# Performance work log

Hardware: AMD Instinct MI355X
Metric: run time of the kernel (lower is better)

The kernel has to match this reference:

```python
import jax, jax.numpy as jnp
import numpy as np

N_NODES = 20000
N_EDGES = 320000
N_GRAPHS = 200
MAX_NODES = 100


def gcn_conv(x, W, b, src, dst, n_nodes):
    # PyG GCNConv: linear transform, add self-loops, symmetric normalization
    h = x @ W                                   # [N, out]
    loop = jnp.arange(n_nodes)
    s = jnp.concatenate([src, loop])
    d = jnp.concatenate([dst, loop])
    deg = jax.ops.segment_sum(jnp.ones_like(s, dtype=h.dtype), d, num_segments=n_nodes)
    dinv = jax.lax.rsqrt(jnp.maximum(deg, 1.0))  # deg >= 1 due to self-loops
    norm = dinv[s] * dinv[d]                     # [E+N]
    msg = h[s] * norm[:, None]                   # gather + scale
    return jax.ops.segment_sum(msg, d, num_segments=n_nodes) + b


def setup_inputs() -> dict:
    key = jax.random.key(0)
    ks = jax.random.split(key, 16)
    IN, H, L = 128, 256, 64
    P = MAX_NODES * (MAX_NODES - 1) // 2
    inp = {
        "x": jax.random.normal(ks[0], (N_NODES, IN), jnp.float32),
        "edge_index": jax.random.randint(ks[1], (2, N_EDGES), 0, N_NODES),
        "batch": jnp.sort(jax.random.randint(ks[2], (N_NODES,), 0, N_GRAPHS)),
        "eps": jax.random.normal(ks[3], (N_GRAPHS, L), jnp.float32),
        "W1": jax.random.normal(ks[4], (IN, H), jnp.float32) * (1.0 / np.sqrt(IN)),
        "b1": jnp.zeros((H,), jnp.float32),
        "W2": jax.random.normal(ks[5], (H, H), jnp.float32) * (1.0 / np.sqrt(H)),
        "b2": jnp.zeros((H,), jnp.float32),
        "Wmu": jax.random.normal(ks[6], (H, L), jnp.float32) * (1.0 / np.sqrt(H)),
        "bmu": jnp.zeros((L,), jnp.float32),
        "Wlv": jax.random.normal(ks[7], (H, L), jnp.float32) * (1.0 / np.sqrt(H)),
        "blv": jnp.zeros((L,), jnp.float32),
        "D1": jax.random.normal(ks[8], (L, H), jnp.float32) * (1.0 / np.sqrt(L)),
        "db1": jnp.zeros((H,), jnp.float32),
        "D2": jax.random.normal(ks[9], (H, H), jnp.float32) * (1.0 / np.sqrt(H)),
        "db2": jnp.zeros((H,), jnp.float32),
        "D3": jax.random.normal(ks[10], (H, P), jnp.float32) * (1.0 / np.sqrt(H)),
        "db3": jnp.zeros((P,), jnp.float32),
    }
    return inp


def reference(x, edge_index, batch, eps, W1, b1, W2, b2, Wmu, bmu, Wlv, blv,
              D1, db1, D2, db2, D3, db3):
    src, dst = edge_index[0], edge_index[1]
    # encoder
    h = jax.nn.relu(gcn_conv(x, W1, b1, src, dst, N_NODES))
    h = jax.nn.relu(gcn_conv(h, W2, b2, src, dst, N_NODES))
    # global mean pool
    sums = jax.ops.segment_sum(h, batch, num_segments=N_GRAPHS)
    cnt = jax.ops.segment_sum(jnp.ones((N_NODES,), h.dtype), batch, num_segments=N_GRAPHS)
    hg = sums / jnp.maximum(cnt, 1.0)[:, None]   # [B, H]
    mu = hg @ Wmu + bmu
    logvar = hg @ Wlv + blv
    # reparameterise
    z = mu + eps * jnp.exp(0.5 * logvar)
    # decoder MLP
    d = jax.nn.relu(z @ D1 + db1)
    d = jax.nn.relu(d @ D2 + db2)
    probs = jax.nn.sigmoid(d @ D3 + db3)         # [B, MAX_NODES*(MAX_NODES-1)//2]
    iu, ju = jnp.triu_indices(MAX_NODES, k=1)
    B = z.shape[0]
    adj = jnp.zeros((B, MAX_NODES, MAX_NODES), probs.dtype)
    adj = adj.at[:, iu, ju].set(probs)
    adj = adj + jnp.swapaxes(adj, 1, 2)
    return adj, mu, logvar
```

## Files before the change

### kernel.cpp

```cpp
#include <hip/hip_runtime.h>
#include <math.h>

#define N_NODES  20000
#define N_EDGES  320000
#define N_GRAPHS 200
#define MAXN     100
#define F_IN     128
#define F_H      256
#define F_L      64
#define P_PAIRS  4950
#define P_PAD    4992
#define ADJ_SIZE (N_GRAPHS * MAXN * MAXN)
#define MU_OFF   ADJ_SIZE
#define LV_OFF   (ADJ_SIZE + N_GRAPHS * F_L)

#define ELL_W    64
#define EF_NB    ((N_EDGES + 255) / 256)

static inline int ceil_div(int a, int b) { return (a + b - 1) / b; }

typedef __attribute__((ext_vector_type(8))) short bf16x8;
typedef __attribute__((ext_vector_type(4))) float f32x4;

static __device__ inline unsigned short f2bf(float f) {
    union { float f; unsigned u; } v; v.f = f;
    unsigned r = (v.u + 0x7FFFu + ((v.u >> 16) & 1u)) >> 16;
    return (unsigned short)r;
}
static __device__ inline float bf2f(unsigned short s) {
    union { unsigned u; float f; } v; v.u = (unsigned)s << 16; return v.f;
}
static __device__ inline float4 ubf4(ushort4 u) {
    float4 f;
    f.x = bf2f(u.x); f.y = bf2f(u.y); f.z = bf2f(u.z); f.w = bf2f(u.w);
    return f;
}
static __device__ inline float rdeg(int d) { return rsqrtf((float)d + 1.0f); }

#define PP_S1  32768
#define PP_S2  98304
#define PP_END 1376256
#define PP_NB  (PP_END / 256)
#define CV_END 640000
#define CV_NB  (CV_END / 256)
__global__ __launch_bounds__(256) void k_prep(
        const int* __restrict__ src, const int* __restrict__ dst,
        int* __restrict__ fill, int* __restrict__ ell,
        const float* __restrict__ W1, const float* __restrict__ W2,
        const float* __restrict__ D3,
        unsigned short* __restrict__ W1p, unsigned short* __restrict__ W2p,
        unsigned short* __restrict__ D3p,
        const float* __restrict__ x, unsigned short* __restrict__ xs) {
    if (blockIdx.x < EF_NB) {
        int e = blockIdx.x * 256 + threadIdx.x;
        if (e < N_EDGES) {
            int d = dst[e];
            int pos = atomicAdd(fill + d, 1);
            if (pos < ELL_W) ell[d * ELL_W + pos] = src[e];
        }
        return;
    }
    if (blockIdx.x < EF_NB + PP_NB) {
        int pid = (blockIdx.x - EF_NB) * 256 + threadIdx.x;
        const float* W; unsigned short* Bp; int N, NP, t;
        if (pid < PP_S1)      { t = pid;          W = W1; Bp = W1p; N = 256;     NP = 256; }
        else if (pid < PP_S2) { t = pid - PP_S1;  W = W2; Bp = W2p; N = 256;     NP = 256; }
        else                  { t = pid - PP_S2;  W = D3; Bp = D3p; N = P_PAIRS; NP = P_PAD; }
        int j    = t & 7;
        int lane = (t >> 3) & 63;
        int tile = t >> 9;
        int NT = NP >> 4;
        int nt = tile % NT;
        int kt = tile / NT;
        int k = kt * 32 + (lane >> 4) * 8 + j;
        int n = nt * 16 + (lane & 15);
        Bp[t] = (n < N) ? f2bf(W[(size_t)k * N + n]) : (unsigned short)0;
        return;
    }
    int tid = (blockIdx.x - EF_NB - PP_NB) * 256 + threadIdx.x;
    if (tid >= CV_END) return;
    float4 val = ((const float4*)x)[tid];
    ushort4 o;
    o.x = f2bf(val.x); o.y = f2bf(val.y);
    o.z = f2bf(val.z); o.w = f2bf(val.w);
    ((ushort4*)xs)[tid] = o;
}

__global__ __launch_bounds__(512) void k_layer1(const unsigned short* __restrict__ xs,
                                                const int* __restrict__ fill,
                                                const int* __restrict__ ell,
                                                const unsigned short* __restrict__ W1p,
                                                const float* __restrict__ bias,
                                                unsigned short* __restrict__ h1s, int M) {
    __shared__ unsigned short At[32 * 128];
    char* Ab = (char*)At;
    const int tid  = threadIdx.x;
    const int lane = tid & 63;
    const int w    = tid >> 6;

    for (int s = 0; s < 4; ++s) {
        int slot = w * 4 + s;
        int v = blockIdx.x * 32 + slot;
        ushort2 ob; ob.x = 0; ob.y = 0;
        if (v < M) {
            int dg  = fill[v];
            int beg = v * ELL_W;
            int end = beg + min(dg, ELL_W);
            float dv = rdeg(dg);
            float2 a0 = make_float2(0.f, 0.f), a1 = make_float2(0.f, 0.f);
            int i = beg;
            for (; i + 8 <= end; i += 8) {
                int s0 = ell[i + 0], s1 = ell[i + 1], s2 = ell[i + 2], s3 = ell[i + 3];
                int s4 = ell[i + 4], s5 = ell[i + 5], s6 = ell[i + 6], s7 = ell[i + 7];
                float r0 = rdeg(fill[s0]), r1 = rdeg(fill[s1]);
                float r2 = rdeg(fill[s2]), r3 = rdeg(fill[s3]);
                float r4 = rdeg(fill[s4]), r5 = rdeg(fill[s5]);
                float r6 = rdeg(fill[s6]), r7 = rdeg(fill[s7]);
                ushort2 u0 = ((const ushort2*)(xs + (size_t)s0 * F_IN))[lane];
                ushort2 u1 = ((const ushort2*)(xs + (size_t)s1 * F_IN))[lane];
                ushort2 u2 = ((const ushort2*)(xs + (size_t)s2 * F_IN))[lane];
                ushort2 u3 = ((const ushort2*)(xs + (size_t)s3 * F_IN))[lane];
                ushort2 u4 = ((const ushort2*)(xs + (size_t)s4 * F_IN))[lane];
                ushort2 u5 = ((const ushort2*)(xs + (size_t)s5 * F_IN))[lane];
                ushort2 u6 = ((const ushort2*)(xs + (size_t)s6 * F_IN))[lane];
                ushort2 u7 = ((const ushort2*)(xs + (size_t)s7 * F_IN))[lane];
                a0.x += r0 * bf2f(u0.x) + r2 * bf2f(u2.x) + r4 * bf2f(u4.x) + r6 * bf2f(u6.x);
                a0.y += r0 * bf2f(u0.y) + r2 * bf2f(u2.y) + r4 * bf2f(u4.y) + r6 * bf2f(u6.y);
                a1.x += r1 * bf2f(u1.x) + r3 * bf2f(u3.x) + r5 * bf2f(u5.x) + r7 * bf2f(u7.x);
                a1.y += r1 * bf2f(u1.y) + r3 * bf2f(u3.y) + r5 * bf2f(u5.y) + r7 * bf2f(u7.y);
            }
            for (; i + 4 <= end; i += 4) {
                int s0 = ell[i + 0], s1 = ell[i + 1], s2 = ell[i + 2], s3 = ell[i + 3];
                float r0 = rdeg(fill[s0]), r1 = rdeg(fill[s1]);
                float r2 = rdeg(fill[s2]), r3 = rdeg(fill[s3]);
                ushort2 u0 = ((const ushort2*)(xs + (size_t)s0 * F_IN))[lane];
                ushort2 u1 = ((const ushort2*)(xs + (size_t)s1 * F_IN))[lane];
                ushort2 u2 = ((const ushort2*)(xs + (size_t)s2 * F_IN))[lane];
                ushort2 u3 = ((const ushort2*)(xs + (size_t)s3 * F_IN))[lane];
                a0.x += r0 * bf2f(u0.x) + r2 * bf2f(u2.x);
                a0.y += r0 * bf2f(u0.y) + r2 * bf2f(u2.y);
                a1.x += r1 * bf2f(u1.x) + r3 * bf2f(u3.x);
                a1.y += r1 * bf2f(u1.y) + r3 * bf2f(u3.y);
            }
            for (; i < end; ++i) {
                int sv = ell[i];
                float rr = rdeg(fill[sv]);
                ushort2 u = ((const ushort2*)(xs + (size_t)sv * F_IN))[lane];
                a0.x += rr * bf2f(u.x); a0.y += rr * bf2f(u.y);
            }
            ushort2 uv = ((const ushort2*)(xs + (size_t)v * F_IN))[lane];
            ob.x = f2bf(dv * (a0.x + a1.x + dv * bf2f(uv.x)));
            ob.y = f2bf(dv * (a0.y + a1.y + dv * bf2f(uv.y)));
        }
        int byteoff = (slot * 256 + lane * 4) ^ ((slot & 7) << 4);
        *(ushort2*)(Ab + byteoff) = ob;
    }
    __syncthreads();

    const int rowhalf = w >> 2;
    const int colgrp  = w & 3;
    const int quad = lane >> 4;
    const int l15  = lane & 15;
    const int ar = rowhalf * 16 + l15;

    f32x4 acc[4];
    #pragma unroll
    for (int nt = 0; nt < 4; ++nt) acc[nt] = (f32x4){0.f, 0.f, 0.f, 0.f};

    #pragma unroll
    for (int kt = 0; kt < 4; ++kt) {
        int c = kt * 64 + quad * 16;
        bf16x8 a0 = *(const bf16x8*)(Ab + ((ar * 256 + c) ^ ((ar & 7) << 4)));
        #pragma unroll
        for (int nt = 0; nt < 4; ++nt) {
            bf16x8 b = *(const bf16x8*)(W1p + (((size_t)kt * 16 + colgrp * 4 + nt) * 64 + lane) * 8);
            acc[nt] = __builtin_amdgcn_mfma_f32_16x16x32_bf16(a0, b, acc[nt], 0, 0, 0);
        }
    }

    #pragma unroll
    for (int r = 0; r < 4; ++r) {
        int gm = blockIdx.x * 32 + rowhalf * 16 + quad * 4 + r;
        if (gm >= M) continue;
        float dv = rdeg(fill[gm]);
        #pragma unroll
        for (int nt = 0; nt < 4; ++nt) {
            int gn = colgrp * 64 + nt * 16 + l15;
            float s = acc[nt][r] + bias[gn];
            h1s[(size_t)gm * F_H + gn] = f2bf(fmaxf(s, 0.0f) * dv);
        }
    }
}

__global__ __launch_bounds__(512) void k_layer2(const unsigned short* __restrict__ h1s,
                                                const int* __restrict__ fill,
                                                const int* __restrict__ ell,
                                                const unsigned short* __restrict__ W2p,
                                                const float* __restrict__ bias,
                                                const int* __restrict__ batch,
                                                float* __restrict__ hg, int M) {
    __shared__ __align__(16) char smem[32 * 260 * 4];
    __shared__ int gb[32];
    char* Ab = smem;
    const int tid  = threadIdx.x;
    const int lane = tid & 63;
    const int w    = tid >> 6;

    if (tid < 32) {
        int gm = blockIdx.x * 32 + tid;
        gb[tid] = (gm < M) ? batch[gm] : -1;
    }

    for (int s = 0; s < 4; ++s) {
        int slot = w * 4 + s;
        int v = blockIdx.x * 32 + slot;
        ushort4 ob; ob.x = ob.y = ob.z = ob.w = 0;
        if (v < M) {
            int dg  = fill[v];
            int beg = v * ELL_W;
            int end = beg + min(dg, ELL_W);
            float4 a0 = make_float4(0.f, 0.f, 0.f, 0.f);
            float4 a1 = make_float4(0.f, 0.f, 0.f, 0.f);
            int i = beg;
            for (; i + 8 <= end; i += 8) {
                int s0 = ell[i + 0], s1 = ell[i + 1], s2 = ell[i + 2], s3 = ell[i + 3];
                int s4 = ell[i + 4], s5 = ell[i + 5], s6 = ell[i + 6], s7 = ell[i + 7];
                float4 h0 = ubf4(((const ushort4*)(h1s + (size_t)s0 * F_H))[lane]);
                float4 h1 = ubf4(((const ushort4*)(h1s + (size_t)s1 * F_H))[lane]);
                float4 h2 = ubf4(((const ushort4*)(h1s + (size_t)s2 * F_H))[lane]);
                float4 h3 = ubf4(((const ushort4*)(h1s + (size_t)s3 * F_H))[lane]);
                float4 h4 = ubf4(((const ushort4*)(h1s + (size_t)s4 * F_H))[lane]);
                float4 h5 = ubf4(((const ushort4*)(h1s + (size_t)s5 * F_H))[lane]);
                float4 h6 = ubf4(((const ushort4*)(h1s + (size_t)s6 * F_H))[lane]);
                float4 h7 = ubf4(((const ushort4*)(h1s + (size_t)s7 * F_H))[lane]);
                a0.x += h0.x + h2.x + h4.x + h6.x; a0.y += h0.y + h2.y + h4.y + h6.y;
                a0.z += h0.z + h2.z + h4.z + h6.z; a0.w += h0.w + h2.w + h4.w + h6.w;
                a1.x += h1.x + h3.x + h5.x + h7.x; a1.y += h1.y + h3.y + h5.y + h7.y;
                a1.z += h1.z + h3.z + h5.z + h7.z; a1.w += h1.w + h3.w + h5.w + h7.w;
            }
            for (; i + 4 <= end; i += 4) {
                int s0 = ell[i + 0], s1 = ell[i + 1], s2 = ell[i + 2], s3 = ell[i + 3];
                float4 h0 = ubf4(((const ushort4*)(h1s + (size_t)s0 * F_H))[lane]);
                float4 h1 = ubf4(((const ushort4*)(h1s + (size_t)s1 * F_H))[lane]);
                float4 h2 = ubf4(((const ushort4*)(h1s + (size_t)s2 * F_H))[lane]);
                float4 h3 = ubf4(((const ushort4*)(h1s + (size_t)s3 * F_H))[lane]);
                a0.x += h0.x + h2.x; a0.y += h0.y + h2.y; a0.z += h0.z + h2.z; a0.w += h0.w + h2.w;
                a1.x += h1.x + h3.x; a1.y += h1.y + h3.y; a1.z += h1.z + h3.z; a1.w += h1.w + h3.w;
            }
            for (; i < end; ++i) {
                int sv = ell[i];
                float4 h = ubf4(((const ushort4*)(h1s + (size_t)sv * F_H))[lane]);
                a0.x += h.x; a0.y += h.y; a0.z += h.z; a0.w += h.w;
            }
            float dv = rdeg(dg);
            float4 hv = ubf4(((const ushort4*)(h1s + (size_t)v * F_H))[lane]);
            ob.x = f2bf(dv * (a0.x + a1.x + hv.x));
            ob.y = f2bf(dv * (a0.y + a1.y + hv.y));
            ob.z = f2bf(dv * (a0.z + a1.z + hv.z));
            ob.w = f2bf(dv * (a0.w + a1.w + hv.w));
        }
        int byteoff = (slot * 512 + lane * 8) ^ ((slot & 7) << 4);
        *(ushort4*)(Ab + byteoff) = ob;
    }
    __syncthreads();

    const int rowhalf = w >> 2;
    const int colgrp  = w & 3;
    const int quad = lane >> 4;
    const int l15  = lane & 15;
    const int ar = rowhalf * 16 + l15;

    f32x4 acc[4];
    #pragma unroll
    for (int nt = 0; nt < 4; ++nt) acc[nt] = (f32x4){0.f, 0.f, 0.f, 0.f};

    #pragma unroll
    for (int kt = 0; kt < 8; ++kt) {
        int cb = kt * 64 + quad * 16;
        bf16x8 a0 = *(const bf16x8*)(Ab + ((ar * 512 + cb) ^ ((ar & 7) << 4)));
        #pragma unroll
        for (int nt = 0; nt < 4; ++nt) {
            bf16x8 b = *(const bf16x8*)(W2p + (((size_t)kt * 16 + colgrp * 4 + nt) * 64 + lane) * 8);
            acc[nt] = __builtin_amdgcn_mfma_f32_16x16x32_bf16(a0, b, acc[nt], 0, 0, 0);
        }
    }
    __syncthreads();

    float* sm = (float*)smem;
    #pragma unroll
    for (int r = 0; r < 4; ++r) {
        int wrow = rowhalf * 16 + quad * 4 + r;
        #pragma unroll
        for (int nt = 0; nt < 4; ++nt) {
            int cl = colgrp * 64 + nt * 16 + l15;
            sm[wrow * 260 + cl] = fmaxf(acc[nt][r] + bias[cl], 0.0f);
        }
    }
    __syncthreads();

    int c  = tid & 255;
    int r0 = (tid >> 8) * 16;
    float s = 0.0f;
    int cur = gb[r0];
    #pragma unroll 4
    for (int r = 0; r < 16; ++r) {
        int g = gb[r0 + r];
        if (g != cur) {
            if (cur >= 0) atomicAdd(hg + (size_t)cur * F_H + c, s);
            s = 0.0f; cur = g;
        }
        s += sm[(r0 + r) * 260 + c];
    }
    if (cur >= 0) atomicAdd(hg + (size_t)cur * F_H + c, s);
}

__global__ __launch_bounds__(512) void k_head_dec(const float* __restrict__ hg,
                                                  const int* __restrict__ batch,
                                                  const float* __restrict__ Wmu,
                                                  const float* __restrict__ bmu,
                                                  const float* __restrict__ Wlv,
                                                  const float* __restrict__ blv,
                                                  const float* __restrict__ eps,
                                                  const float* __restrict__ D1,
                                                  const float* __restrict__ db1,
                                                  const float* __restrict__ D2,
                                                  const float* __restrict__ db2,
                                                  float* __restrict__ out,
                                                  unsigned short* __restrict__ d2b) {
    int g = blockIdx.x;
    int tid = threadIdx.x;
    __shared__ float hgs[F_H];
    __shared__ float pp[512];
    __shared__ float mulv[128];
    __shared__ float zs[F_L];
    __shared__ float d1s[F_H];
    __shared__ float sInv;
    if (tid == 0) {
        int lo = 0, hi = N_NODES;
        while (lo < hi) { int mid = (lo + hi) >> 1; if (batch[mid] < g) lo = mid + 1; else hi = mid; }
        int beg = lo;
        hi = N_NODES;
        while (lo < hi) { int mid = (lo + hi) >> 1; if (batch[mid] < g + 1) lo = mid + 1; else hi = mid; }
        sInv = 1.0f / fmaxf((float)(lo - beg), 1.0f);
    }
    __syncthreads();
    if (tid < F_H) hgs[tid] = hg[(size_t)g * F_H + tid] * sInv;
    __syncthreads();
    {
        int o = tid & 127;
        int q = tid >> 7;
        int l = o & 63;
        const float* W = (o < 64) ? Wmu : Wlv;
        float s = 0.0f;
        int k0 = q * 64;
        #pragma unroll 8
        for (int k = k0; k < k0 + 64; ++k) s += hgs[k] * W[(size_t)k * F_L + l];
        pp[tid] = s;
    }
    __syncthreads();
    if (tid < 128) {
        int l = tid & 63;
        float s = pp[tid] + pp[tid + 128] + pp[tid + 256] + pp[tid + 384]
                + ((tid < 64) ? bmu[l] : blv[l]);
        out[((tid < 64) ? MU_OFF : LV_OFF) + g * F_L + l] = s;
        mulv[tid] = s;
    }
    __syncthreads();
    if (tid < 64)
        zs[tid] = mulv[tid] + eps[g * F_L + tid] * expf(0.5f * mulv[64 + tid]);
    __syncthreads();
    {
        int o = tid & 255;
        int h = tid >> 8;
        float s = 0.0f;
        int k0 = h * 32;
        #pragma unroll 8
        for (int k = k0; k < k0 + 32; ++k) s += zs[k] * D1[(size_t)k * F_H + o];
        pp[tid] = s;
    }
    __syncthreads();
    if (tid < 256) d1s[tid] = fmaxf(pp[tid] + pp[tid + 256] + db1[tid], 0.0f);
    __syncthreads();
    {
        int o = tid & 255;
        int h = tid >> 8;
        float s = 0.0f;
        int k0 = h * 128;
        #pragma unroll 8
        for (int k = k0; k < k0 + 128; ++k) s += d1s[k] * D2[(size_t)k * F_H + o];
        pp[tid] = s;
    }
    __syncthreads();
    if (tid < 256)
        d2b[(size_t)g * F_H + tid] = f2bf(fmaxf(pp[tid] + pp[tid + 256] + db2[tid], 0.0f));
}

__global__ __launch_bounds__(256) void k_gemm3(const unsigned short* __restrict__ A,
                                               const unsigned short* __restrict__ Bp,
                                               float* __restrict__ Y,
                                               const float* __restrict__ bias,
                                               int M, int N, int NP) {
    constexpr int KT = F_H / 32;
    const int NT   = NP >> 4;
    const int lane = threadIdx.x & 63;
    const int wave = threadIdx.x >> 6;
    const int bm   = blockIdx.y * 32;
    const int ng   = blockIdx.x * 4 + wave;
    const int quad = lane >> 4;
    const int l15  = lane & 15;

    int m0 = bm + l15;
    int m1 = m0 + 16;
    int m0c = min(m0, M - 1), m1c = min(m1, M - 1);

    f32x4 acc[2];
    acc[0] = (f32x4){0.f, 0.f, 0.f, 0.f};
    acc[1] = (f32x4){0.f, 0.f, 0.f, 0.f};

    #pragma unroll
    for (int kt = 0; kt < KT; ++kt) {
        bf16x8 a0 = *(const bf16x8*)(A + (size_t)m0c * F_H + kt * 32 + quad * 8);
        bf16x8 a1 = *(const bf16x8*)(A + (size_t)m1c * F_H + kt * 32 + quad * 8);
        bf16x8 b = *(const bf16x8*)(Bp + (((size_t)kt * NT + ng) * 64 + lane) * 8);
        acc[0] = __builtin_amdgcn_mfma_f32_16x16x32_bf16(a0, b, acc[0], 0, 0, 0);
        acc[1] = __builtin_amdgcn_mfma_f32_16x16x32_bf16(a1, b, acc[1], 0, 0, 0);
    }

    #pragma unroll
    for (int i = 0; i < 2; ++i) {
        #pragma unroll
        for (int r = 0; r < 4; ++r) {
            int gm = bm + i * 16 + quad * 4 + r;
            if (gm >= M) continue;
            int gn = (ng << 4) + l15;
            if (gn >= N) continue;
            float s = acc[i][r] + bias[gn];
            Y[(size_t)gm * N + gn] = 1.0f / (1.0f + expf(-s));
        }
    }
}

__global__ __launch_bounds__(256) void k_adj(const float* __restrict__ probs,
                                             float* __restrict__ adj) {
    int i = blockIdx.x * blockDim.x + threadIdx.x;
    if (i >= N_GRAPHS * MAXN * (MAXN / 4)) return;
    int b4 = (i % (MAXN / 4)) * 4;
    int a  = (i / (MAXN / 4)) % MAXN;
    int g  = i / (MAXN * (MAXN / 4));
    const float* pg = probs + (size_t)g * P_PAIRS;
    float4 o;
    float* op = (float*)&o;
    #pragma unroll
    for (int c = 0; c < 4; ++c) {
        int b = b4 + c;
        float v = 0.0f;
        if (a != b) {
            int lo = min(a, b), hi = max(a, b);
            int p = lo * (MAXN - 1) - (lo * (lo - 1)) / 2 + (hi - lo - 1);
            v = pg[p];
        }
        op[c] = v;
    }
    ((float4*)adj)[i] = o;
}

extern "C" void kernel_launch(void* const* d_in, const int* in_sizes, int n_in,
                              void* d_out, int out_size, void* d_ws, size_t ws_size,
                              hipStream_t stream) {
    const float* x    = (const float*)d_in[0];
    const int*   eidx = (const int*)d_in[1];
    const int*   batch= (const int*)d_in[2];
    const float* eps  = (const float*)d_in[3];
    const float* W1   = (const float*)d_in[4];
    const float* b1   = (const float*)d_in[5];
    const float* W2   = (const float*)d_in[6];
    const float* b2   = (const float*)d_in[7];
    const float* Wmu  = (const float*)d_in[8];
    const float* bmu  = (const float*)d_in[9];
    const float* Wlv  = (const float*)d_in[10];
    const float* blv  = (const float*)d_in[11];
    const float* D1   = (const float*)d_in[12];
    const float* db1  = (const float*)d_in[13];
    const float* D2   = (const float*)d_in[14];
    const float* db2  = (const float*)d_in[15];
    const float* D3   = (const float*)d_in[16];
    const float* db3  = (const float*)d_in[17];

    const int* src = eidx;
    const int* dst = eidx + N_EDGES;
    float* out = (float*)d_out;

    char* wsb = (char*)d_ws;
    size_t o = 0;
    auto carve = [&](size_t bytes) { void* p = wsb + o; o += (bytes + 255) & ~255ull; return p; };
    int*   fill   = (int*)  carve(N_NODES * sizeof(int));
    float* hg     = (float*)carve((size_t)N_GRAPHS * F_H * sizeof(float));
    int*   ell    = (int*)  carve((size_t)N_NODES * ELL_W * sizeof(int));
    unsigned short* xs  = (unsigned short*)carve((size_t)N_NODES * F_IN * sizeof(short));
    unsigned short* W1p = (unsigned short*)carve((size_t)F_IN * F_H * sizeof(short));
    unsigned short* W2p = (unsigned short*)carve((size_t)F_H * F_H * sizeof(short));
    unsigned short* D3p = (unsigned short*)carve((size_t)F_H * P_PAD * sizeof(short));
    unsigned short* h1s = (unsigned short*)carve((size_t)N_NODES * F_H * sizeof(short));
    unsigned short* d2b = (unsigned short*)carve((size_t)N_GRAPHS * F_H * sizeof(short));
    float* probs  = (float*)carve((size_t)N_GRAPHS * P_PAIRS * sizeof(float));

    hipMemsetAsync(fill, 0, 284928, stream);
    k_prep<<<EF_NB + PP_NB + CV_NB, 256, 0, stream>>>(src, dst, fill, ell,
                                                      W1, W2, D3, W1p, W2p, D3p,
                                                      x, xs);

    k_layer1<<<ceil_div(N_NODES, 32), 512, 0, stream>>>(xs, fill, ell,
                                                        W1p, b1, h1s, N_NODES);

    k_layer2<<<ceil_div(N_NODES, 32), 512, 0, stream>>>(h1s, fill, ell,
                                                        W2p, b2, batch, hg, N_NODES);

    k_head_dec<<<N_GRAPHS, 512, 0, stream>>>(hg, batch, Wmu, bmu, Wlv, blv, eps,
                                             D1, db1, D2, db2, out, d2b);

    {
        dim3 grid(P_PAD / 64, ceil_div(N_GRAPHS, 32));
        k_gemm3<<<grid, 256, 0, stream>>>(d2b, D3p, probs, db3,
                                          N_GRAPHS, P_PAIRS, P_PAD);
    }

    k_adj<<<ceil_div(N_GRAPHS * MAXN * (MAXN / 4), 256), 256, 0, stream>>>(probs, out);
}
```

Before: 207.6 us.

## Halve node tile per block in GCN layers to 16 rows and store pooled rows as bf16

Layer1 and layer2 now handle 16 nodes per 512-thread block instead of 32, doubling the grid. Each wave gathers 2 nodes instead of 4 and computes a 16x32 output slice with 2 MFMA accumulators. This trades more blocks and more repeated weight-fragment loads for shorter per-block gather latency and better load balance across CUs. Layer2 also stages the ReLU output in LDS as bf16 with a 272-short row stride, so the shared buffer shrinks. This adds rounding before the mean-pool atomics.

```diff
diff --git a/kernel.cpp b/kernel.cpp
--- a/kernel.cpp
+++ b/kernel.cpp
@@ -92,15 +92,15 @@
                                                 const unsigned short* __restrict__ W1p,
                                                 const float* __restrict__ bias,
                                                 unsigned short* __restrict__ h1s, int M) {
-    __shared__ unsigned short At[32 * 128];
+    __shared__ unsigned short At[16 * 128];
     char* Ab = (char*)At;
     const int tid  = threadIdx.x;
     const int lane = tid & 63;
     const int w    = tid >> 6;
 
-    for (int s = 0; s < 4; ++s) {
-        int slot = w * 4 + s;
-        int v = blockIdx.x * 32 + slot;
+    for (int s = 0; s < 2; ++s) {
+        int slot = w * 2 + s;
+        int v = blockIdx.x * 16 + slot;
         ushort2 ob; ob.x = 0; ob.y = 0;
         if (v < M) {
             int dg  = fill[v];
@@ -157,35 +157,33 @@
     }
     __syncthreads();
 
-    const int rowhalf = w >> 2;
-    const int colgrp  = w & 3;
     const int quad = lane >> 4;
     const int l15  = lane & 15;
-    const int ar = rowhalf * 16 + l15;
-
-    f32x4 acc[4];
-    #pragma unroll
-    for (int nt = 0; nt < 4; ++nt) acc[nt] = (f32x4){0.f, 0.f, 0.f, 0.f};
+    const int ar = l15;
+
+    f32x4 acc[2];
+    acc[0] = (f32x4){0.f, 0.f, 0.f, 0.f};
+    acc[1] = (f32x4){0.f, 0.f, 0.f, 0.f};
 
     #pragma unroll
     for (int kt = 0; kt < 4; ++kt) {
         int c = kt * 64 + quad * 16;
         bf16x8 a0 = *(const bf16x8*)(Ab + ((ar * 256 + c) ^ ((ar & 7) << 4)));
         #pragma unroll
-        for (int nt = 0; nt < 4; ++nt) {
-            bf16x8 b = *(const bf16x8*)(W1p + (((size_t)kt * 16 + colgrp * 4 + nt) * 64 + lane) * 8);
+        for (int nt = 0; nt < 2; ++nt) {
+            bf16x8 b = *(const bf16x8*)(W1p + (((size_t)kt * 16 + w * 2 + nt) * 64 + lane) * 8);
             acc[nt] = __builtin_amdgcn_mfma_f32_16x16x32_bf16(a0, b, acc[nt], 0, 0, 0);
         }
     }
 
     #pragma unroll
     for (int r = 0; r < 4; ++r) {
-        int gm = blockIdx.x * 32 + rowhalf * 16 + quad * 4 + r;
+        int gm = blockIdx.x * 16 + quad * 4 + r;
         if (gm >= M) continue;
         float dv = rdeg(fill[gm]);
         #pragma unroll
-        for (int nt = 0; nt < 4; ++nt) {
-            int gn = colgrp * 64 + nt * 16 + l15;
+        for (int nt = 0; nt < 2; ++nt) {
+            int gn = w * 32 + nt * 16 + l15;
             float s = acc[nt][r] + bias[gn];
             h1s[(size_t)gm * F_H + gn] = f2bf(fmaxf(s, 0.0f) * dv);
         }
@@ -199,21 +197,21 @@
                                                 const float* __restrict__ bias,
                                                 const int* __restrict__ batch,
                                                 float* __restrict__ hg, int M) {
-    __shared__ __align__(16) char smem[32 * 260 * 4];
-    __shared__ int gb[32];
+    __shared__ __align__(16) char smem[16 * 272 * 2];
+    __shared__ int gb[16];
     char* Ab = smem;
     const int tid  = threadIdx.x;
     const int lane = tid & 63;
     const int w    = tid >> 6;
 
-    if (tid < 32) {
-        int gm = blockIdx.x * 32 + tid;
+    if (tid < 16) {
+        int gm = blockIdx.x * 16 + tid;
         gb[tid] = (gm < M) ? batch[gm] : -1;
     }
 
-    for (int s = 0; s < 4; ++s) {
-        int slot = w * 4 + s;
-        int v = blockIdx.x * 32 + slot;
+    for (int s = 0; s < 2; ++s) {
+        int slot = w * 2 + s;
+        int v = blockIdx.x * 16 + slot;
         ushort4 ob; ob.x = ob.y = ob.z = ob.w = 0;
         if (v < M) {
             int dg  = fill[v];
@@ -264,52 +262,50 @@
     }
     __syncthreads();
 
-    const int rowhalf = w >> 2;
-    const int colgrp  = w & 3;
     const int quad = lane >> 4;
     const int l15  = lane & 15;
-    const int ar = rowhalf * 16 + l15;
-
-    f32x4 acc[4];
-    #pragma unroll
-    for (int nt = 0; nt < 4; ++nt) acc[nt] = (f32x4){0.f, 0.f, 0.f, 0.f};
+    const int ar = l15;
+
+    f32x4 acc[2];
+    acc[0] = (f32x4){0.f, 0.f, 0.f, 0.f};
+    acc[1] = (f32x4){0.f, 0.f, 0.f, 0.f};
 
     #pragma unroll
     for (int kt = 0; kt < 8; ++kt) {
         int cb = kt * 64 + quad * 16;
         bf16x8 a0 = *(const bf16x8*)(Ab + ((ar * 512 + cb) ^ ((ar & 7) << 4)));
         #pragma unroll
-        for (int nt = 0; nt < 4; ++nt) {
-            bf16x8 b = *(const bf16x8*)(W2p + (((size_t)kt * 16 + colgrp * 4 + nt) * 64 + lane) * 8);
+        for (int nt = 0; nt < 2; ++nt) {
+            bf16x8 b = *(const bf16x8*)(W2p + (((size_t)kt * 16 + w * 2 + nt) * 64 + lane) * 8);
             acc[nt] = __builtin_amdgcn_mfma_f32_16x16x32_bf16(a0, b, acc[nt], 0, 0, 0);
         }
     }
     __syncthreads();
 
-    float* sm = (float*)smem;
+    unsigned short* sm = (unsigned short*)smem;
     #pragma unroll
     for (int r = 0; r < 4; ++r) {
-        int wrow = rowhalf * 16 + quad * 4 + r;
+        int wrow = quad * 4 + r;
         #pragma unroll
-        for (int nt = 0; nt < 4; ++nt) {
-            int cl = colgrp * 64 + nt * 16 + l15;
-            sm[wrow * 260 + cl] = fmaxf(acc[nt][r] + bias[cl], 0.0f);
+        for (int nt = 0; nt < 2; ++nt) {
+            int cl = w * 32 + nt * 16 + l15;
+            sm[wrow * 272 + cl] = f2bf(fmaxf(acc[nt][r] + bias[cl], 0.0f));
         }
     }
     __syncthreads();
 
     int c  = tid & 255;
-    int r0 = (tid >> 8) * 16;
+    int r0 = (tid >> 8) * 8;
     float s = 0.0f;
     int cur = gb[r0];
     #pragma unroll 4
-    for (int r = 0; r < 16; ++r) {
+    for (int r = 0; r < 8; ++r) {
         int g = gb[r0 + r];
         if (g != cur) {
             if (cur >= 0) atomicAdd(hg + (size_t)cur * F_H + c, s);
             s = 0.0f; cur = g;
         }
-        s += sm[(r0 + r) * 260 + c];
+        s += bf2f(sm[(r0 + r) * 272 + c]);
     }
     if (cur >= 0) atomicAdd(hg + (size_t)cur * F_H + c, s);
 }
@@ -509,10 +505,10 @@
                                                       W1, W2, D3, W1p, W2p, D3p,
                                                       x, xs);
 
-    k_layer1<<<ceil_div(N_NODES, 32), 512, 0, stream>>>(xs, fill, ell,
+    k_layer1<<<ceil_div(N_NODES, 16), 512, 0, stream>>>(xs, fill, ell,
                                                         W1p, b1, h1s, N_NODES);
 
-    k_layer2<<<ceil_div(N_NODES, 32), 512, 0, stream>>>(h1s, fill, ell,
+    k_layer2<<<ceil_div(N_NODES, 16), 512, 0, stream>>>(h1s, fill, ell,
                                                         W2p, b2, batch, hg, N_NODES);
 
     k_head_dec<<<N_GRAPHS, 512, 0, stream>>>(hg, batch, Wmu, bmu, Wlv, blv, eps,
```

Result: no change. 204.7 us (-1.4%).
